# Kernel optimization log

Measured on AMD Instinct MI355X. Metric: run time of the kernel, lower is better.

The kernel has to match this reference:

```python
import jax, jax.numpy as jnp
import numpy as np

B, SQ, SK = 2, 2048, 4096
D_STATE, D_LISTEN, D_PROJ, H = 512, 512, 512, 8


def setup_inputs() -> dict:
    key = jax.random.key(0)
    ks = jax.random.split(key, 9)
    s = 0.02
    return {
        "q": jax.random.normal(ks[0], (B, SQ, D_STATE), jnp.float32),
        "k": jax.random.normal(ks[1], (B, SK, D_LISTEN), jnp.float32),
        "mask": jax.random.randint(ks[2], (B, SK), 0, 2, jnp.int32),
        "Wq": jax.random.normal(ks[3], (D_STATE, D_PROJ), jnp.float32) * s,
        "bq": jnp.zeros((D_PROJ,), jnp.float32),
        "Wk": jax.random.normal(ks[4], (D_LISTEN, D_PROJ), jnp.float32) * s,
        "bk": jnp.zeros((D_PROJ,), jnp.float32),
        "Wv": jax.random.normal(ks[5], (D_LISTEN, D_PROJ), jnp.float32) * s,
        "bv": jnp.zeros((D_PROJ,), jnp.float32),
    }


def reference(q, k, mask, Wq, bq, Wk, bk, Wv, bv):
    # projections
    qp = q @ Wq + bq                      # [B, SQ, D]
    kp = k @ Wk + bk                      # [B, SK, D]
    vp = k @ Wv + bv                      # [B, SK, D]
    W = D_PROJ // H                        # head width
    qh = qp.reshape(B, SQ, H, W).transpose(0, 2, 1, 3)  # [B,H,SQ,W]
    kh = kp.reshape(B, SK, H, W).transpose(0, 2, 1, 3)  # [B,H,SK,W]
    vh = vp.reshape(B, SK, H, W).transpose(0, 2, 1, 3)  # [B,H,SK,W]
    scores = jnp.einsum("bhqw,bhkw->bhqk", qh, kh) / np.sqrt(W).astype(np.float32)
    m = mask[:, None, None, :].astype(jnp.float32)       # [B,1,1,SK]
    scores = scores - 10000.0 * (1.0 - m)
    attn = jax.nn.softmax(scores, axis=-1)               # dropout=0 (eval)
    h = jnp.einsum("bhqk,bhkw->bhqw", attn, vh)          # [B,H,SQ,W]
    h = h.transpose(0, 2, 1, 3).reshape(B, SQ, D_PROJ)
    return h
```

## Files before the change

### kernel.cpp

```cpp
#include <hip/hip_runtime.h>
#include <hip/hip_bf16.h>


typedef short  s16x8 __attribute__((ext_vector_type(8)));
typedef short  s16x4 __attribute__((ext_vector_type(4)));
typedef float  f32x4 __attribute__((ext_vector_type(4)));
typedef float  f32x16 __attribute__((ext_vector_type(16)));
typedef unsigned int u32;
typedef unsigned int u32x4 __attribute__((ext_vector_type(4)));

__device__ __forceinline__ unsigned short f2bf(float x) {
    return __builtin_bit_cast(unsigned short, __float2bfloat16(x));
}
__device__ __forceinline__ void gload16(const void* g, void* lds) {
    __builtin_amdgcn_global_load_lds(
        (const __attribute__((address_space(1))) unsigned int*)g,
        (__attribute__((address_space(3))) unsigned int*)lds, 16, 0, 0);
}
__device__ __forceinline__ u32 cvtpk(float lo, float hi) {
    u32 r;
    asm("v_cvt_pk_bf16_f32 %0, %1, %2" : "=v"(r) : "v"(lo), "v"(hi));
    return r;
}

__global__ __launch_bounds__(256) void prep(
    const float* __restrict__ q, const float* __restrict__ k,
    const float* __restrict__ Wq, const float* __restrict__ Wk,
    const float* __restrict__ Wv, const int* __restrict__ mask,
    unsigned short* __restrict__ qbf, unsigned short* __restrict__ kbf,
    unsigned short* __restrict__ wtq, unsigned short* __restrict__ wtk,
    unsigned short* __restrict__ wtv, int* __restrict__ cntb)
{
    __shared__ float T[64][65];
    const int bid = blockIdx.x;
    const int tid = threadIdx.x;
    if (bid < 3072) {
        const float* src = bid < 1024 ? q : k;
        unsigned short* dst = bid < 1024 ? qbf : kbf;
        int i = (bid < 1024 ? bid : bid - 1024) * 256 + tid;
        float4 a = reinterpret_cast<const float4*>(src)[2 * i];
        float4 b = reinterpret_cast<const float4*>(src)[2 * i + 1];
        s16x8 o;
        o[0] = (short)f2bf(a.x); o[1] = (short)f2bf(a.y);
        o[2] = (short)f2bf(a.z); o[3] = (short)f2bf(a.w);
        o[4] = (short)f2bf(b.x); o[5] = (short)f2bf(b.y);
        o[6] = (short)f2bf(b.z); o[7] = (short)f2bf(b.w);
        reinterpret_cast<s16x8*>(dst)[i] = o;
    } else if (bid < 3264) {
        int t = bid - 3072;
        int z = t >> 6;
        int tt = t & 63;
        const float* W = z == 0 ? Wq : z == 1 ? Wk : Wv;
        unsigned short* D = z == 0 ? wtq : z == 1 ? wtk : wtv;
        const int k0 = (tt >> 3) * 64, n0 = (tt & 7) * 64;
        const int r = tid >> 2, cq = tid & 3;
        #pragma unroll
        for (int p = 0; p < 4; ++p) {
            int c = (cq + 4 * p) * 4;
            float4 v = *reinterpret_cast<const float4*>(
                &W[(size_t)(k0 + r) * 512 + n0 + c]);
            T[c + 0][r] = v.x; T[c + 1][r] = v.y;
            T[c + 2][r] = v.z; T[c + 3][r] = v.w;
        }
        __syncthreads();
        #pragma unroll
        for (int p = 0; p < 4; ++p) {
            int kc = (cq + 4 * p) * 4;
            s16x4 o;
            o[0] = (short)f2bf(T[r][kc + 0]);
            o[1] = (short)f2bf(T[r][kc + 1]);
            o[2] = (short)f2bf(T[r][kc + 2]);
            o[3] = (short)f2bf(T[r][kc + 3]);
            *reinterpret_cast<s16x4*>(&D[(size_t)(n0 + r) * 512 + k0 + kc]) = o;
        }
    } else {
        __shared__ int red[4];
        int b = bid - 3264;
        int base = b * 4096 + tid * 16;
        int s = 0;
        #pragma unroll
        for (int p = 0; p < 4; ++p) {
            int4 m = *reinterpret_cast<const int4*>(&mask[base + 4 * p]);
            s += m.x + m.y + m.z + m.w;
        }
        #pragma unroll
        for (int off = 1; off < 64; off <<= 1)
            s += __shfl_xor(s, off);
        if ((tid & 63) == 0) red[tid >> 6] = s;
        __syncthreads();
        if (tid == 0)
            cntb[b] = 4096 - (red[0] + red[1] + red[2] + red[3]);
    }
}

__global__ __launch_bounds__(256) void proj3(
    const unsigned short* __restrict__ qbf, const unsigned short* __restrict__ kbf,
    const unsigned short* __restrict__ wtq, const unsigned short* __restrict__ wtk,
    const unsigned short* __restrict__ wtv,
    const float* __restrict__ bq, const float* __restrict__ bk,
    const float* __restrict__ bv, const int* __restrict__ mask,
    unsigned short* __restrict__ qh, unsigned short* __restrict__ kh,
    unsigned short* __restrict__ vt)
{
    __shared__ unsigned short As[2][128 * 64];
    __shared__ unsigned short Bs[2][64 * 64];

    const int tid  = threadIdx.x;
    const int wv   = tid >> 6;
    const int lane = tid & 63;
    const int g    = lane >> 4;
    const int ln   = lane & 15;
    const int swz  = (ln & 7) << 3;

    const int id = blockIdx.x;
    const unsigned short *A, *Wt;
    const float* bias;
    unsigned short* dst;
    int S, trans, nb, mb, mflag;
    if (id < 256)      { A = qbf; Wt = wtq; bias = bq; dst = qh; S = 2048; trans = 0; mflag = 0; nb = id & 7;         mb = id >> 3; }
    else if (id < 768) { A = kbf; Wt = wtk; bias = bk; dst = kh; S = 4096; trans = 0; mflag = 1; nb = (id - 256) & 7; mb = (id - 256) >> 3; }
    else               { A = kbf; Wt = wtv; bias = bv; dst = vt; S = 4096; trans = 1; mflag = 2; nb = (id - 768) & 7; mb = (id - 768) >> 3; }
    const int m0 = mb * 128, n0 = nb * 64;
    const float scl = (mflag == 0) ? 0.18033688011112042f : 1.f;

    f32x4 acc[4][2];
    #pragma unroll
    for (int i = 0; i < 4; ++i)
        #pragma unroll
        for (int j = 0; j < 2; ++j) acc[i][j] = (f32x4)0.f;

    auto stage = [&](int bufn, int k0) {
        #pragma unroll
        for (int p = 0; p < 4; ++p) {
            int slot = p * 256 + tid;
            int row = slot >> 3, cb = slot & 7;
            int cbp = cb ^ (row & 7);
            gload16(&A[(size_t)(m0 + row) * 512 + k0 + cbp * 8], &As[bufn][slot * 8]);
        }
        #pragma unroll
        for (int p = 0; p < 2; ++p) {
            int slot = p * 256 + tid;
            int row = slot >> 3, cb = slot & 7;
            int cbp = cb ^ (row & 7);
            gload16(&Wt[(size_t)(n0 + row) * 512 + k0 + cbp * 8], &Bs[bufn][slot * 8]);
        }
    };

    stage(0, 0);
    __syncthreads();
    int buf = 0;
    for (int kk = 0; kk < 8; ++kk) {
        if (kk < 7) stage(buf ^ 1, (kk + 1) * 64);
        #pragma unroll
        for (int ks = 0; ks < 2; ++ks) {
            s16x8 fa[2], fb[4];
            #pragma unroll
            for (int mi = 0; mi < 2; ++mi)
                fa[mi] = *reinterpret_cast<const s16x8*>(
                    &As[buf][((wv * 32 + 16 * mi + ln) * 64 + ks * 32 + g * 8) ^ swz]);
            #pragma unroll
            for (int nj = 0; nj < 4; ++nj)
                fb[nj] = *reinterpret_cast<const s16x8*>(
                    &Bs[buf][((16 * nj + ln) * 64 + ks * 32 + g * 8) ^ swz]);
            if (!trans) {
                #pragma unroll
                for (int mi = 0; mi < 2; ++mi)
                    #pragma unroll
                    for (int nj = 0; nj < 4; ++nj)
                        acc[nj][mi] = __builtin_amdgcn_mfma_f32_16x16x32_bf16(
                            fa[mi], fb[nj], acc[nj][mi], 0, 0, 0);
            } else {
                #pragma unroll
                for (int nj = 0; nj < 4; ++nj)
                    #pragma unroll
                    for (int mi = 0; mi < 2; ++mi)
                        acc[nj][mi] = __builtin_amdgcn_mfma_f32_16x16x32_bf16(
                            fb[nj], fa[mi], acc[nj][mi], 0, 0, 0);
            }
        }
        __syncthreads();
        buf ^= 1;
    }

    const int h    = nb;
    const int bidx = m0 / S;
    const int s0   = m0 - bidx * S;

    if (!trans) {
        float bvv[4];
        #pragma unroll
        for (int nj = 0; nj < 4; ++nj) bvv[nj] = bias[n0 + 16 * nj + ln];
        unsigned short* base = dst + (size_t)(bidx * 8 + h) * S * 64;
        #pragma unroll
        for (int mi = 0; mi < 2; ++mi)
            #pragma unroll
            for (int r = 0; r < 4; ++r) {
                int s = s0 + wv * 32 + 16 * mi + 4 * g + r;
                float fm = (mflag == 1) ? (float)mask[bidx * 4096 + s] : 1.f;
                float fs = fm * scl;
                #pragma unroll
                for (int nj = 0; nj < 4; ++nj)
                    base[(size_t)s * 64 + 16 * nj + ln] =
                        f2bf((acc[nj][mi][r] + bvv[nj]) * fs);
            }
    } else {
        float fmc[2];
        #pragma unroll
        for (int mi = 0; mi < 2; ++mi)
            fmc[mi] = (float)mask[bidx * 4096 + s0 + wv * 32 + 16 * mi + ln];
        unsigned short* base = dst + (size_t)(bidx * 8 + h) * 64 * (size_t)S;
        #pragma unroll
        for (int nj = 0; nj < 4; ++nj)
            #pragma unroll
            for (int r = 0; r < 4; ++r) {
                int w = 16 * nj + 4 * g + r;
                float bw = bias[n0 + w];
                #pragma unroll
                for (int mi = 0; mi < 2; ++mi)
                    base[(size_t)w * S + s0 + wv * 32 + 16 * mi + ln] =
                        f2bf((acc[nj][mi][r] + bw) * fmc[mi]);
            }
    }
}

__global__ __launch_bounds__(512) void attn11(
    const unsigned short* __restrict__ qh,
    const unsigned short* __restrict__ kh,
    const unsigned short* __restrict__ vt,
    const int* __restrict__ cntb,
    float* __restrict__ out)
{
    __shared__ float Ored[2][4][32][36];
    __shared__ float lw[2][2][4][32];

    const int tid  = threadIdx.x;
    const int wid  = tid >> 6;
    const int kq   = wid & 3;
    const int qg   = wid >> 2;
    const int lane = tid & 63;
    const int l31  = lane & 31;
    const int h32  = lane >> 5;

    const int id  = blockIdx.x;
    const int xcd = id & 7;
    const int j   = id >> 3;
    const int bh  = xcd * 2 + (j >> 4);
    const int qt  = j & 15;
    const int b   = bh >> 3;
    const int hh  = bh & 7;

    const unsigned short* Kp = kh + (size_t)bh * 4096 * 64
                               + (size_t)(kq * 32 + l31) * 64 + h32 * 8;
    const unsigned short* Vp0 = vt + (size_t)bh * 64 * 4096
                               + (size_t)l31 * 4096 + kq * 32 + h32 * 8;

    s16x8 Qf[2][4];
    {
        const unsigned short* Qb = qh + ((size_t)bh * 2048 + qt * 128 + qg * 64) * 64;
        #pragma unroll
        for (int qt2 = 0; qt2 < 2; ++qt2)
            #pragma unroll
            for (int ks = 0; ks < 4; ++ks)
                Qf[qt2][ks] = *reinterpret_cast<const s16x8*>(
                    &Qb[(size_t)(qt2 * 32 + l31) * 64 + ks * 16 + h32 * 8]);
    }

    f32x16 O[2][2];
    #pragma unroll
    for (int i = 0; i < 2; ++i)
        #pragma unroll
        for (int jj = 0; jj < 2; ++jj) O[i][jj] = (f32x16)0.f;
    float l_acc0 = 0.f, l_acc1 = 0.f;

    s16x8 kf[4], vf[4];

    auto loadK = [&](int t) {
        #pragma unroll
        for (int ks = 0; ks < 4; ++ks)
            kf[ks] = *reinterpret_cast<const s16x8*>(Kp + (size_t)t * 8192 + ks * 16);
    };
    auto loadV = [&](int t) {
        #pragma unroll
        for (int wt = 0; wt < 2; ++wt)
            #pragma unroll
            for (int t2 = 0; t2 < 2; ++t2)
                vf[wt * 2 + t2] = *reinterpret_cast<const s16x8*>(
                    Vp0 + (size_t)wt * 32 * 4096 + t * 128 + t2 * 16);
    };

    loadK(0); loadV(0);

    for (int t = 0; t < 32; ++t) {
        f32x16 S[2];
        S[0] = (f32x16)0.f; S[1] = (f32x16)0.f;
        __builtin_amdgcn_s_setprio(1);
        #pragma unroll
        for (int ks = 0; ks < 4; ++ks) {
            S[0] = __builtin_amdgcn_mfma_f32_32x32x16_bf16(kf[ks], Qf[0][ks], S[0], 0, 0, 0);
            S[1] = __builtin_amdgcn_mfma_f32_32x32x16_bf16(kf[ks], Qf[1][ks], S[1], 0, 0, 0);
        }
        __builtin_amdgcn_s_setprio(0);
        if (t < 31) loadK(t + 1);

        s16x8 pa[2][2];
        #pragma unroll
        for (int qt2 = 0; qt2 < 2; ++qt2) {
            float pp[16];
            #pragma unroll
            for (int r = 0; r < 16; ++r)
                pp[r] = exp2f(S[qt2][r]);
            float ls = (((pp[0] + pp[1]) + (pp[2] + pp[3]))
                     + ((pp[4] + pp[5]) + (pp[6] + pp[7])))
                     + (((pp[8] + pp[9]) + (pp[10] + pp[11]))
                     + ((pp[12] + pp[13]) + (pp[14] + pp[15])));
            if (qt2 == 0) l_acc0 += ls; else l_acc1 += ls;
            u32 W[8];
            #pragma unroll
            for (int c = 0; c < 4; ++c) {
                W[2 * c + 0] = cvtpk(pp[4 * c + 0], pp[4 * c + 1]);
                W[2 * c + 1] = cvtpk(pp[4 * c + 2], pp[4 * c + 3]);
            }
            asm("v_permlane32_swap_b32 %0, %1" : "+v"(W[0]), "+v"(W[2]));
            asm("v_permlane32_swap_b32 %0, %1" : "+v"(W[1]), "+v"(W[3]));
            asm("v_permlane32_swap_b32 %0, %1" : "+v"(W[4]), "+v"(W[6]));
            asm("v_permlane32_swap_b32 %0, %1" : "+v"(W[5]), "+v"(W[7]));
            u32x4 lo, hi;
            lo[0] = W[0]; lo[1] = W[1]; lo[2] = W[2]; lo[3] = W[3];
            hi[0] = W[4]; hi[1] = W[5]; hi[2] = W[6]; hi[3] = W[7];
            pa[qt2][0] = __builtin_bit_cast(s16x8, lo);
            pa[qt2][1] = __builtin_bit_cast(s16x8, hi);
        }

        __builtin_amdgcn_s_setprio(1);
        #pragma unroll
        for (int qt2 = 0; qt2 < 2; ++qt2)
            #pragma unroll
            for (int wt = 0; wt < 2; ++wt)
                #pragma unroll
                for (int t2 = 0; t2 < 2; ++t2)
                    O[qt2][wt] = __builtin_amdgcn_mfma_f32_32x32x16_bf16(
                        pa[qt2][t2], vf[wt * 2 + t2], O[qt2][wt], 0, 0, 0);
        __builtin_amdgcn_s_setprio(0);
        if (t < 31) loadV(t + 1);
    }

    float ls0 = l_acc0 + __shfl_xor(l_acc0, 32);
    float ls1 = l_acc1 + __shfl_xor(l_acc1, 32);
    if (lane < 32) {
        lw[qg][0][kq][l31] = ls0;
        lw[qg][1][kq][l31] = ls1;
    }

    const float cnt = (float)cntb[b];
    const int grp = tid >> 8;
    const int tt  = tid & 255;
    const int qr  = tt >> 3;
    const int w8  = (tt & 7) * 4;
    #pragma unroll
    for (int qt2 = 0; qt2 < 2; ++qt2)
        #pragma unroll
        for (int wt = 0; wt < 2; ++wt) {
            __syncthreads();
            f32x16 oo = O[qt2][wt];
            #pragma unroll
            for (int r = 0; r < 16; ++r)
                Ored[qg][kq][(r & 3) + 8 * (r >> 2) + 4 * h32][l31] = oo[r];
            __syncthreads();
            float4 s  = *reinterpret_cast<const float4*>(&Ored[grp][0][qr][w8]);
            float4 s1 = *reinterpret_cast<const float4*>(&Ored[grp][1][qr][w8]);
            float4 s2 = *reinterpret_cast<const float4*>(&Ored[grp][2][qr][w8]);
            float4 s3 = *reinterpret_cast<const float4*>(&Ored[grp][3][qr][w8]);
            float l = (lw[grp][qt2][0][qr] + lw[grp][qt2][1][qr]
                     + lw[grp][qt2][2][qr] + lw[grp][qt2][3][qr]) - cnt;
            float inv = 1.f / l;
            int qglob = qt * 128 + grp * 64 + qt2 * 32 + qr;
            float4 o;
            o.x = (s.x + s1.x + s2.x + s3.x) * inv;
            o.y = (s.y + s1.y + s2.y + s3.y) * inv;
            o.z = (s.z + s1.z + s2.z + s3.z) * inv;
            o.w = (s.w + s1.w + s2.w + s3.w) * inv;
            *reinterpret_cast<float4*>(
                &out[((size_t)b * 2048 + qglob) * 512 + hh * 64 + wt * 32 + w8]) = o;
        }
}

extern "C" void kernel_launch(void* const* d_in, const int* in_sizes, int n_in,
                              void* d_out, int out_size, void* d_ws, size_t ws_size,
                              hipStream_t stream)
{
    const float* q    = (const float*)d_in[0];
    const float* k    = (const float*)d_in[1];
    const int*   mask = (const int*)  d_in[2];
    const float* Wq   = (const float*)d_in[3];
    const float* bq   = (const float*)d_in[4];
    const float* Wk   = (const float*)d_in[5];
    const float* bk   = (const float*)d_in[6];
    const float* Wv   = (const float*)d_in[7];
    const float* bv   = (const float*)d_in[8];
    float* out = (float*)d_out;

    unsigned short* p = (unsigned short*)d_ws;
    unsigned short* qh  = p; p += (size_t)2 * 8 * 2048 * 64;
    unsigned short* kh  = p; p += (size_t)2 * 8 * 4096 * 64;
    unsigned short* vt  = p; p += (size_t)2 * 8 * 4096 * 64;
    unsigned short* qbf = p; p += (size_t)2 * 2048 * 512;
    unsigned short* kbf = p; p += (size_t)2 * 4096 * 512;
    unsigned short* wtq = p; p += 512 * 512;
    unsigned short* wtk = p; p += 512 * 512;
    unsigned short* wtv = p; p += 512 * 512;
    int* cntb = (int*)p;

    dim3 blk(256);
    prep<<<dim3(3266), blk, 0, stream>>>(q, k, Wq, Wk, Wv, mask,
                                         qbf, kbf, wtq, wtk, wtv, cntb);
    proj3<<<dim3(1280), blk, 0, stream>>>(qbf, kbf, wtq, wtk, wtv,
                                          bq, bk, bv, mask, qh, kh, vt);
    attn11<<<dim3(256), dim3(512), 0, stream>>>(qh, kh, vt, cntb, out);
}
```

Measured before the change: 106.4 us.

## Software-pipeline attention loop: overlap next QK MFMA with current softmax

Restructures the attention inner loop into a two-stage software pipeline with ping-pong score buffers, so the QK^T MFMAs for the next key tile are issued before the exp/convert softmax work of the current tile. This aims to hide transcendental and pack latency behind matrix-core work. It also sets launch bounds to one block per CU, letting the compiler use more registers for the extra live score and probability buffers. The doubled register footprint risks spills, and the changed load ordering may alter memory latency hiding.

```diff
diff --git a/kernel.cpp b/kernel.cpp
--- a/kernel.cpp
+++ b/kernel.cpp
@@ -223,7 +223,7 @@
     }
 }
 
-__global__ __launch_bounds__(512) void attn11(
+__global__ __launch_bounds__(512, 1) void attn12(
     const unsigned short* __restrict__ qh,
     const unsigned short* __restrict__ kh,
     const unsigned short* __restrict__ vt,
@@ -287,28 +287,23 @@
                 vf[wt * 2 + t2] = *reinterpret_cast<const s16x8*>(
                     Vp0 + (size_t)wt * 32 * 4096 + t * 128 + t2 * 16);
     };
-
-    loadK(0); loadV(0);
-
-    for (int t = 0; t < 32; ++t) {
-        f32x16 S[2];
-        S[0] = (f32x16)0.f; S[1] = (f32x16)0.f;
+    auto QK = [&](f32x16* Sv) {
+        Sv[0] = (f32x16)0.f; Sv[1] = (f32x16)0.f;
         __builtin_amdgcn_s_setprio(1);
         #pragma unroll
         for (int ks = 0; ks < 4; ++ks) {
-            S[0] = __builtin_amdgcn_mfma_f32_32x32x16_bf16(kf[ks], Qf[0][ks], S[0], 0, 0, 0);
-            S[1] = __builtin_amdgcn_mfma_f32_32x32x16_bf16(kf[ks], Qf[1][ks], S[1], 0, 0, 0);
+            Sv[0] = __builtin_amdgcn_mfma_f32_32x32x16_bf16(kf[ks], Qf[0][ks], Sv[0], 0, 0, 0);
+            Sv[1] = __builtin_amdgcn_mfma_f32_32x32x16_bf16(kf[ks], Qf[1][ks], Sv[1], 0, 0, 0);
         }
         __builtin_amdgcn_s_setprio(0);
-        if (t < 31) loadK(t + 1);
-
-        s16x8 pa[2][2];
+    };
+    auto SM = [&](const f32x16* Sv, s16x8 pa[2][2]) {
         #pragma unroll
         for (int qt2 = 0; qt2 < 2; ++qt2) {
             float pp[16];
             #pragma unroll
             for (int r = 0; r < 16; ++r)
-                pp[r] = exp2f(S[qt2][r]);
+                pp[r] = exp2f(Sv[qt2][r]);
             float ls = (((pp[0] + pp[1]) + (pp[2] + pp[3]))
                      + ((pp[4] + pp[5]) + (pp[6] + pp[7])))
                      + (((pp[8] + pp[9]) + (pp[10] + pp[11]))
@@ -330,7 +325,8 @@
             pa[qt2][0] = __builtin_bit_cast(s16x8, lo);
             pa[qt2][1] = __builtin_bit_cast(s16x8, hi);
         }
-
+    };
+    auto PV = [&](s16x8 pa[2][2]) {
         __builtin_amdgcn_s_setprio(1);
         #pragma unroll
         for (int qt2 = 0; qt2 < 2; ++qt2)
@@ -341,7 +337,28 @@
                     O[qt2][wt] = __builtin_amdgcn_mfma_f32_32x32x16_bf16(
                         pa[qt2][t2], vf[wt * 2 + t2], O[qt2][wt], 0, 0, 0);
         __builtin_amdgcn_s_setprio(0);
-        if (t < 31) loadV(t + 1);
+    };
+
+    f32x16 SA[2], SB[2];
+    s16x8 paA[2][2], paB[2][2];
+
+    loadK(0);
+    QK(SA);
+    loadK(1);
+    loadV(0);
+
+    for (int tt = 0; tt < 16; ++tt) {
+        const int t0 = 2 * tt;
+        QK(SB);
+        if (t0 + 2 < 32) loadK(t0 + 2);
+        SM(SA, paA);
+        PV(paA);
+        loadV(t0 + 1);
+        if (t0 + 2 < 32) QK(SA);
+        if (t0 + 3 < 32) loadK(t0 + 3);
+        SM(SB, paB);
+        PV(paB);
+        if (t0 + 2 < 32) loadV(t0 + 2);
     }
 
     float ls0 = l_acc0 + __shfl_xor(l_acc0, 32);
@@ -415,5 +432,5 @@
                                          qbf, kbf, wtq, wtk, wtv, cntb);
     proj3<<<dim3(1280), blk, 0, stream>>>(qbf, kbf, wtq, wtk, wtv,
                                           bq, bk, bv, mask, qh, kh, vt);
-    attn11<<<dim3(256), dim3(512), 0, stream>>>(qh, kh, vt, cntb, out);
-}
+    attn12<<<dim3(256), dim3(512), 0, stream>>>(qh, kh, vt, cntb, out);
+}
```

Measured after the change: 115.4 us. 8.5% more time.

## Fuse fp32-to-bf16 conversion of q and k into projection GEMM staging

Applied to the files above, without the earlier changes.

The separate prep pass that converted q and k to bf16 in workspace is removed. The projection kernel now loads fp32 activations into registers, converts them, and writes the swizzled bf16 tile to LDS after the MFMA loop, keeping double buffering. This drops one full read and write of the activations plus their workspace, but each K tile is now read twice as fp32 (for the K and V projections) and costs more register pressure and conversion ALU work inside the GEMM.

```diff
diff --git a/kernel.cpp b/kernel.cpp
--- a/kernel.cpp
+++ b/kernel.cpp
@@ -24,32 +24,17 @@
 }
 
 __global__ __launch_bounds__(256) void prep(
-    const float* __restrict__ q, const float* __restrict__ k,
     const float* __restrict__ Wq, const float* __restrict__ Wk,
     const float* __restrict__ Wv, const int* __restrict__ mask,
-    unsigned short* __restrict__ qbf, unsigned short* __restrict__ kbf,
     unsigned short* __restrict__ wtq, unsigned short* __restrict__ wtk,
     unsigned short* __restrict__ wtv, int* __restrict__ cntb)
 {
     __shared__ float T[64][65];
     const int bid = blockIdx.x;
     const int tid = threadIdx.x;
-    if (bid < 3072) {
-        const float* src = bid < 1024 ? q : k;
-        unsigned short* dst = bid < 1024 ? qbf : kbf;
-        int i = (bid < 1024 ? bid : bid - 1024) * 256 + tid;
-        float4 a = reinterpret_cast<const float4*>(src)[2 * i];
-        float4 b = reinterpret_cast<const float4*>(src)[2 * i + 1];
-        s16x8 o;
-        o[0] = (short)f2bf(a.x); o[1] = (short)f2bf(a.y);
-        o[2] = (short)f2bf(a.z); o[3] = (short)f2bf(a.w);
-        o[4] = (short)f2bf(b.x); o[5] = (short)f2bf(b.y);
-        o[6] = (short)f2bf(b.z); o[7] = (short)f2bf(b.w);
-        reinterpret_cast<s16x8*>(dst)[i] = o;
-    } else if (bid < 3264) {
-        int t = bid - 3072;
-        int z = t >> 6;
-        int tt = t & 63;
+    if (bid < 192) {
+        int z = bid >> 6;
+        int tt = bid & 63;
         const float* W = z == 0 ? Wq : z == 1 ? Wk : Wv;
         unsigned short* D = z == 0 ? wtq : z == 1 ? wtk : wtv;
         const int k0 = (tt >> 3) * 64, n0 = (tt & 7) * 64;
@@ -75,7 +60,7 @@
         }
     } else {
         __shared__ int red[4];
-        int b = bid - 3264;
+        int b = bid - 192;
         int base = b * 4096 + tid * 16;
         int s = 0;
         #pragma unroll
@@ -94,7 +79,7 @@
 }
 
 __global__ __launch_bounds__(256) void proj3(
-    const unsigned short* __restrict__ qbf, const unsigned short* __restrict__ kbf,
+    const float* __restrict__ qf, const float* __restrict__ kf,
     const unsigned short* __restrict__ wtq, const unsigned short* __restrict__ wtk,
     const unsigned short* __restrict__ wtv,
     const float* __restrict__ bq, const float* __restrict__ bk,
@@ -113,13 +98,14 @@
     const int swz  = (ln & 7) << 3;
 
     const int id = blockIdx.x;
-    const unsigned short *A, *Wt;
+    const float* A;
+    const unsigned short* Wt;
     const float* bias;
     unsigned short* dst;
     int S, trans, nb, mb, mflag;
-    if (id < 256)      { A = qbf; Wt = wtq; bias = bq; dst = qh; S = 2048; trans = 0; mflag = 0; nb = id & 7;         mb = id >> 3; }
-    else if (id < 768) { A = kbf; Wt = wtk; bias = bk; dst = kh; S = 4096; trans = 0; mflag = 1; nb = (id - 256) & 7; mb = (id - 256) >> 3; }
-    else               { A = kbf; Wt = wtv; bias = bv; dst = vt; S = 4096; trans = 1; mflag = 2; nb = (id - 768) & 7; mb = (id - 768) >> 3; }
+    if (id < 256)      { A = qf; Wt = wtq; bias = bq; dst = qh; S = 2048; trans = 0; mflag = 0; nb = id & 7;         mb = id >> 3; }
+    else if (id < 768) { A = kf; Wt = wtk; bias = bk; dst = kh; S = 4096; trans = 0; mflag = 1; nb = (id - 256) & 7; mb = (id - 256) >> 3; }
+    else               { A = kf; Wt = wtv; bias = bv; dst = vt; S = 4096; trans = 1; mflag = 2; nb = (id - 768) & 7; mb = (id - 768) >> 3; }
     const int m0 = mb * 128, n0 = nb * 64;
     const float scl = (mflag == 0) ? 0.18033688011112042f : 1.f;
 
@@ -129,14 +115,33 @@
         #pragma unroll
         for (int j = 0; j < 2; ++j) acc[i][j] = (f32x4)0.f;
 
-    auto stage = [&](int bufn, int k0) {
+    float4 Ar[4][2];
+
+    auto issueA = [&](int k0) {
         #pragma unroll
         for (int p = 0; p < 4; ++p) {
-            int slot = p * 256 + tid;
-            int row = slot >> 3, cb = slot & 7;
+            int gslot = p * 256 + tid;
+            int row = gslot >> 3, cb = gslot & 7;
             int cbp = cb ^ (row & 7);
-            gload16(&A[(size_t)(m0 + row) * 512 + k0 + cbp * 8], &As[bufn][slot * 8]);
-        }
+            const float* src = &A[(size_t)(m0 + row) * 512 + k0 + cbp * 8];
+            Ar[p][0] = *reinterpret_cast<const float4*>(src);
+            Ar[p][1] = *reinterpret_cast<const float4*>(src + 4);
+        }
+    };
+    auto writeA = [&](int bufn) {
+        #pragma unroll
+        for (int p = 0; p < 4; ++p) {
+            int gslot = p * 256 + tid;
+            int row = gslot >> 3, cb = gslot & 7;
+            s16x8 o;
+            o[0] = (short)f2bf(Ar[p][0].x); o[1] = (short)f2bf(Ar[p][0].y);
+            o[2] = (short)f2bf(Ar[p][0].z); o[3] = (short)f2bf(Ar[p][0].w);
+            o[4] = (short)f2bf(Ar[p][1].x); o[5] = (short)f2bf(Ar[p][1].y);
+            o[6] = (short)f2bf(Ar[p][1].z); o[7] = (short)f2bf(Ar[p][1].w);
+            *reinterpret_cast<s16x8*>(&As[bufn][row * 64 + cb * 8]) = o;
+        }
+    };
+    auto stageW = [&](int bufn, int k0) {
         #pragma unroll
         for (int p = 0; p < 2; ++p) {
             int slot = p * 256 + tid;
@@ -146,11 +151,17 @@
         }
     };
 
-    stage(0, 0);
+    issueA(0);
+    stageW(0, 0);
+    writeA(0);
     __syncthreads();
+
     int buf = 0;
     for (int kk = 0; kk < 8; ++kk) {
-        if (kk < 7) stage(buf ^ 1, (kk + 1) * 64);
+        if (kk < 7) {
+            issueA((kk + 1) * 64);
+            stageW(buf ^ 1, (kk + 1) * 64);
+        }
         #pragma unroll
         for (int ks = 0; ks < 2; ++ks) {
             s16x8 fa[2], fb[4];
@@ -178,6 +189,7 @@
                             fb[nj], fa[mi], acc[nj][mi], 0, 0, 0);
             }
         }
+        if (kk < 7) writeA(buf ^ 1);
         __syncthreads();
         buf ^= 1;
     }
@@ -403,17 +415,15 @@
     unsigned short* qh  = p; p += (size_t)2 * 8 * 2048 * 64;
     unsigned short* kh  = p; p += (size_t)2 * 8 * 4096 * 64;
     unsigned short* vt  = p; p += (size_t)2 * 8 * 4096 * 64;
-    unsigned short* qbf = p; p += (size_t)2 * 2048 * 512;
-    unsigned short* kbf = p; p += (size_t)2 * 4096 * 512;
     unsigned short* wtq = p; p += 512 * 512;
     unsigned short* wtk = p; p += 512 * 512;
     unsigned short* wtv = p; p += 512 * 512;
     int* cntb = (int*)p;
 
     dim3 blk(256);
-    prep<<<dim3(3266), blk, 0, stream>>>(q, k, Wq, Wk, Wv, mask,
-                                         qbf, kbf, wtq, wtk, wtv, cntb);
-    proj3<<<dim3(1280), blk, 0, stream>>>(qbf, kbf, wtq, wtk, wtv,
+    prep<<<dim3(194), blk, 0, stream>>>(Wq, Wk, Wv, mask,
+                                        wtq, wtk, wtv, cntb);
+    proj3<<<dim3(1280), blk, 0, stream>>>(q, k, wtq, wtk, wtv,
                                           bq, bk, bv, mask, qh, kh, vt);
     attn11<<<dim3(256), dim3(512), 0, stream>>>(qh, kh, vt, cntb, out);
 }
```

Result: slower. 124.8 us (+17.3%).

## Enlarge projection GEMM tiles and compute softmax row sums via MFMA

Applied to the files above, without the earlier changes.

The projection kernel moves from 128x64 to 128x128 output tiles, with each wave computing a 64x64 sub-tile. This halves the block count and raises operand reuse per LDS load, at the cost of more accumulator registers and more LDS. In the attention kernel, the scalar VALU summation of exp values into the softmax denominator is replaced by an extra MFMA against a vector of bf16 ones. That moves the sum onto the matrix units but rounds the summed probabilities to bf16 and adds two MFMAs per tile.

```diff
diff --git a/kernel.cpp b/kernel.cpp
--- a/kernel.cpp
+++ b/kernel.cpp
@@ -93,7 +93,7 @@
     }
 }
 
-__global__ __launch_bounds__(256) void proj3(
+__global__ __launch_bounds__(256) void proj4(
     const unsigned short* __restrict__ qbf, const unsigned short* __restrict__ kbf,
     const unsigned short* __restrict__ wtq, const unsigned short* __restrict__ wtk,
     const unsigned short* __restrict__ wtv,
@@ -103,7 +103,7 @@
     unsigned short* __restrict__ vt)
 {
     __shared__ unsigned short As[2][128 * 64];
-    __shared__ unsigned short Bs[2][64 * 64];
+    __shared__ unsigned short Bs[2][128 * 64];
 
     const int tid  = threadIdx.x;
     const int wv   = tid >> 6;
@@ -111,23 +111,25 @@
     const int g    = lane >> 4;
     const int ln   = lane & 15;
     const int swz  = (ln & 7) << 3;
+    const int r0   = (wv >> 1) * 64;
+    const int c0   = (wv & 1) * 64;
 
     const int id = blockIdx.x;
     const unsigned short *A, *Wt;
     const float* bias;
     unsigned short* dst;
     int S, trans, nb, mb, mflag;
-    if (id < 256)      { A = qbf; Wt = wtq; bias = bq; dst = qh; S = 2048; trans = 0; mflag = 0; nb = id & 7;         mb = id >> 3; }
-    else if (id < 768) { A = kbf; Wt = wtk; bias = bk; dst = kh; S = 4096; trans = 0; mflag = 1; nb = (id - 256) & 7; mb = (id - 256) >> 3; }
-    else               { A = kbf; Wt = wtv; bias = bv; dst = vt; S = 4096; trans = 1; mflag = 2; nb = (id - 768) & 7; mb = (id - 768) >> 3; }
-    const int m0 = mb * 128, n0 = nb * 64;
+    if (id < 128)      { A = qbf; Wt = wtq; bias = bq; dst = qh; S = 2048; trans = 0; mflag = 0; nb = id & 3;         mb = id >> 2; }
+    else if (id < 384) { A = kbf; Wt = wtk; bias = bk; dst = kh; S = 4096; trans = 0; mflag = 1; nb = (id - 128) & 3; mb = (id - 128) >> 2; }
+    else               { A = kbf; Wt = wtv; bias = bv; dst = vt; S = 4096; trans = 1; mflag = 2; nb = (id - 384) & 3; mb = (id - 384) >> 2; }
+    const int m0 = mb * 128, n0 = nb * 128;
     const float scl = (mflag == 0) ? 0.18033688011112042f : 1.f;
 
-    f32x4 acc[4][2];
+    f32x4 acc[4][4];
     #pragma unroll
     for (int i = 0; i < 4; ++i)
         #pragma unroll
-        for (int j = 0; j < 2; ++j) acc[i][j] = (f32x4)0.f;
+        for (int j = 0; j < 4; ++j) acc[i][j] = (f32x4)0.f;
 
     auto stage = [&](int bufn, int k0) {
         #pragma unroll
@@ -138,7 +140,7 @@
             gload16(&A[(size_t)(m0 + row) * 512 + k0 + cbp * 8], &As[bufn][slot * 8]);
         }
         #pragma unroll
-        for (int p = 0; p < 2; ++p) {
+        for (int p = 0; p < 4; ++p) {
             int slot = p * 256 + tid;
             int row = slot >> 3, cb = slot & 7;
             int cbp = cb ^ (row & 7);
@@ -153,77 +155,77 @@
         if (kk < 7) stage(buf ^ 1, (kk + 1) * 64);
         #pragma unroll
         for (int ks = 0; ks < 2; ++ks) {
-            s16x8 fa[2], fb[4];
-            #pragma unroll
-            for (int mi = 0; mi < 2; ++mi)
+            s16x8 fa[4], fb[4];
+            #pragma unroll
+            for (int mi = 0; mi < 4; ++mi)
                 fa[mi] = *reinterpret_cast<const s16x8*>(
-                    &As[buf][((wv * 32 + 16 * mi + ln) * 64 + ks * 32 + g * 8) ^ swz]);
+                    &As[buf][((r0 + 16 * mi + ln) * 64 + ks * 32 + g * 8) ^ swz]);
             #pragma unroll
             for (int nj = 0; nj < 4; ++nj)
                 fb[nj] = *reinterpret_cast<const s16x8*>(
-                    &Bs[buf][((16 * nj + ln) * 64 + ks * 32 + g * 8) ^ swz]);
+                    &Bs[buf][((c0 + 16 * nj + ln) * 64 + ks * 32 + g * 8) ^ swz]);
             if (!trans) {
                 #pragma unroll
-                for (int mi = 0; mi < 2; ++mi)
+                for (int mi = 0; mi < 4; ++mi)
                     #pragma unroll
                     for (int nj = 0; nj < 4; ++nj)
-                        acc[nj][mi] = __builtin_amdgcn_mfma_f32_16x16x32_bf16(
-                            fa[mi], fb[nj], acc[nj][mi], 0, 0, 0);
+                        acc[mi][nj] = __builtin_amdgcn_mfma_f32_16x16x32_bf16(
+                            fa[mi], fb[nj], acc[mi][nj], 0, 0, 0);
             } else {
                 #pragma unroll
-                for (int nj = 0; nj < 4; ++nj)
+                for (int mi = 0; mi < 4; ++mi)
                     #pragma unroll
-                    for (int mi = 0; mi < 2; ++mi)
-                        acc[nj][mi] = __builtin_amdgcn_mfma_f32_16x16x32_bf16(
-                            fb[nj], fa[mi], acc[nj][mi], 0, 0, 0);
+                    for (int nj = 0; nj < 4; ++nj)
+                        acc[mi][nj] = __builtin_amdgcn_mfma_f32_16x16x32_bf16(
+                            fb[nj], fa[mi], acc[mi][nj], 0, 0, 0);
             }
         }
         __syncthreads();
         buf ^= 1;
     }
 
-    const int h    = nb;
+    const int head = nb * 2 + (c0 >> 6);
     const int bidx = m0 / S;
     const int s0   = m0 - bidx * S;
 
     if (!trans) {
         float bvv[4];
         #pragma unroll
-        for (int nj = 0; nj < 4; ++nj) bvv[nj] = bias[n0 + 16 * nj + ln];
-        unsigned short* base = dst + (size_t)(bidx * 8 + h) * S * 64;
-        #pragma unroll
-        for (int mi = 0; mi < 2; ++mi)
+        for (int nj = 0; nj < 4; ++nj) bvv[nj] = bias[n0 + c0 + 16 * nj + ln];
+        unsigned short* base = dst + (size_t)(bidx * 8 + head) * S * 64;
+        #pragma unroll
+        for (int mi = 0; mi < 4; ++mi)
             #pragma unroll
             for (int r = 0; r < 4; ++r) {
-                int s = s0 + wv * 32 + 16 * mi + 4 * g + r;
+                int s = s0 + r0 + 16 * mi + 4 * g + r;
                 float fm = (mflag == 1) ? (float)mask[bidx * 4096 + s] : 1.f;
                 float fs = fm * scl;
                 #pragma unroll
                 for (int nj = 0; nj < 4; ++nj)
                     base[(size_t)s * 64 + 16 * nj + ln] =
-                        f2bf((acc[nj][mi][r] + bvv[nj]) * fs);
+                        f2bf((acc[mi][nj][r] + bvv[nj]) * fs);
             }
     } else {
-        float fmc[2];
-        #pragma unroll
-        for (int mi = 0; mi < 2; ++mi)
-            fmc[mi] = (float)mask[bidx * 4096 + s0 + wv * 32 + 16 * mi + ln];
-        unsigned short* base = dst + (size_t)(bidx * 8 + h) * 64 * (size_t)S;
+        float fmc[4];
+        #pragma unroll
+        for (int mi = 0; mi < 4; ++mi)
+            fmc[mi] = (float)mask[bidx * 4096 + s0 + r0 + 16 * mi + ln];
+        unsigned short* base = dst + (size_t)(bidx * 8 + head) * 64 * (size_t)S;
         #pragma unroll
         for (int nj = 0; nj < 4; ++nj)
             #pragma unroll
             for (int r = 0; r < 4; ++r) {
-                int w = 16 * nj + 4 * g + r;
-                float bw = bias[n0 + w];
+                int wl = 16 * nj + 4 * g + r;
+                float bw = bias[n0 + c0 + wl];
                 #pragma unroll
-                for (int mi = 0; mi < 2; ++mi)
-                    base[(size_t)w * S + s0 + wv * 32 + 16 * mi + ln] =
-                        f2bf((acc[nj][mi][r] + bw) * fmc[mi]);
+                for (int mi = 0; mi < 4; ++mi)
+                    base[(size_t)wl * S + s0 + r0 + 16 * mi + ln] =
+                        f2bf((acc[mi][nj][r] + bw) * fmc[mi]);
             }
     }
 }
 
-__global__ __launch_bounds__(512) void attn11(
+__global__ __launch_bounds__(512) void attn16(
     const unsigned short* __restrict__ qh,
     const unsigned short* __restrict__ kh,
     const unsigned short* __restrict__ vt,
@@ -265,12 +267,17 @@
                     &Qb[(size_t)(qt2 * 32 + l31) * 64 + ks * 16 + h32 * 8]);
     }
 
-    f32x16 O[2][2];
+    f32x16 O[2][2], Ol[2];
     #pragma unroll
-    for (int i = 0; i < 2; ++i)
+    for (int i = 0; i < 2; ++i) {
+        Ol[i] = (f32x16)0.f;
         #pragma unroll
         for (int jj = 0; jj < 2; ++jj) O[i][jj] = (f32x16)0.f;
-    float l_acc0 = 0.f, l_acc1 = 0.f;
+    }
+
+    s16x8 ones;
+    #pragma unroll
+    for (int i = 0; i < 8; ++i) ones[i] = (short)0x3F80;
 
     s16x8 kf[4], vf[4];
 
@@ -309,11 +316,6 @@
             #pragma unroll
             for (int r = 0; r < 16; ++r)
                 pp[r] = exp2f(S[qt2][r]);
-            float ls = (((pp[0] + pp[1]) + (pp[2] + pp[3]))
-                     + ((pp[4] + pp[5]) + (pp[6] + pp[7])))
-                     + (((pp[8] + pp[9]) + (pp[10] + pp[11]))
-                     + ((pp[12] + pp[13]) + (pp[14] + pp[15])));
-            if (qt2 == 0) l_acc0 += ls; else l_acc1 += ls;
             u32 W[8];
             #pragma unroll
             for (int c = 0; c < 4; ++c) {
@@ -333,22 +335,28 @@
 
         __builtin_amdgcn_s_setprio(1);
         #pragma unroll
-        for (int qt2 = 0; qt2 < 2; ++qt2)
+        for (int qt2 = 0; qt2 < 2; ++qt2) {
             #pragma unroll
             for (int wt = 0; wt < 2; ++wt)
                 #pragma unroll
                 for (int t2 = 0; t2 < 2; ++t2)
                     O[qt2][wt] = __builtin_amdgcn_mfma_f32_32x32x16_bf16(
                         pa[qt2][t2], vf[wt * 2 + t2], O[qt2][wt], 0, 0, 0);
+            #pragma unroll
+            for (int t2 = 0; t2 < 2; ++t2)
+                Ol[qt2] = __builtin_amdgcn_mfma_f32_32x32x16_bf16(
+                    pa[qt2][t2], ones, Ol[qt2], 0, 0, 0);
+        }
         __builtin_amdgcn_s_setprio(0);
         if (t < 31) loadV(t + 1);
     }
 
-    float ls0 = l_acc0 + __shfl_xor(l_acc0, 32);
-    float ls1 = l_acc1 + __shfl_xor(l_acc1, 32);
-    if (lane < 32) {
-        lw[qg][0][kq][l31] = ls0;
-        lw[qg][1][kq][l31] = ls1;
+    if (l31 == 0) {
+        #pragma unroll
+        for (int qt2 = 0; qt2 < 2; ++qt2)
+            #pragma unroll
+            for (int r = 0; r < 16; ++r)
+                lw[qg][qt2][kq][(r & 3) + 8 * (r >> 2) + 4 * h32] = Ol[qt2][r];
     }
 
     const float cnt = (float)cntb[b];
@@ -413,7 +421,7 @@
     dim3 blk(256);
     prep<<<dim3(3266), blk, 0, stream>>>(q, k, Wq, Wk, Wv, mask,
                                          qbf, kbf, wtq, wtk, wtv, cntb);
-    proj3<<<dim3(1280), blk, 0, stream>>>(qbf, kbf, wtq, wtk, wtv,
-                                          bq, bk, bv, mask, qh, kh, vt);
-    attn11<<<dim3(256), dim3(512), 0, stream>>>(qh, kh, vt, cntb, out);
-}
+    proj4<<<dim3(640), blk, 0, stream>>>(qbf, kbf, wtq, wtk, wtv,
+                                         bq, bk, bv, mask, qh, kh, vt);
+    attn16<<<dim3(256), dim3(512), 0, stream>>>(qh, kh, vt, cntb, out);
+}
```

Result: faster. 97.70 us (-8.2%).
